# Kernel tuning notes

Hardware: AMD Instinct MI355X
Metric: run time of the kernel (lower is better)

Reference implementation:

```python
import jax, jax.numpy as jnp
import numpy as np

L, H, D, DH, F = 2, 12, 768, 64, 3072
B, T = 2, 2048
LN_EPS = 1e-5


def setup_inputs() -> dict:
    key = jax.random.key(0)
    ks = jax.random.split(key, 16)
    s = 0.02
    inp = {
        "x": jax.random.normal(ks[0], (B, T, D), dtype=jnp.float32),
        "attn_mask": jnp.ones((1, T, T), dtype=jnp.int32),
        # per-layer, per-head QKV projections
        "Wq": jax.random.normal(ks[1], (L, H, D, DH), jnp.float32) * s,
        "bq": jnp.zeros((L, H, DH), jnp.float32),
        "Wk": jax.random.normal(ks[2], (L, H, D, DH), jnp.float32) * s,
        "bk": jnp.zeros((L, H, DH), jnp.float32),
        "Wv": jax.random.normal(ks[3], (L, H, D, DH), jnp.float32) * s,
        "bv": jnp.zeros((L, H, DH), jnp.float32),
        # output projection over concatenated heads
        "Wo": jax.random.normal(ks[4], (L, H * DH, D), jnp.float32) * s,
        "bo": jnp.zeros((L, D), jnp.float32),
        # FFN: LayerNorm -> Linear -> GELU -> Linear
        "ln_g": jnp.ones((L, D), jnp.float32),
        "ln_b": jnp.zeros((L, D), jnp.float32),
        "W1": jax.random.normal(ks[5], (L, D, F), jnp.float32) * s,
        "b1": jnp.zeros((L, F), jnp.float32),
        "W2": jax.random.normal(ks[6], (L, F, D), jnp.float32) * s,
        "b2": jnp.zeros((L, D), jnp.float32),
    }
    return inp


def _layer(x, mask, Wq, bq, Wk, bk, Wv, bv, Wo, bo, ln_g, ln_b, W1, b1, W2, b2):
    # batched multi-head attention (equivalent to per-head loop in source)
    q = jnp.einsum("btd,hde->bhte", x, Wq) + bq[None, :, None, :]
    k = jnp.einsum("btd,hde->bhte", x, Wk) + bk[None, :, None, :]
    v = jnp.einsum("btd,hde->bhte", x, Wv) + bv[None, :, None, :]
    scores = jnp.einsum("bhte,bhse->bhts", q, k) / np.sqrt(DH).astype(np.float32)
    scores = jnp.where(mask[:, None, :, :] == 0, -jnp.inf, scores)
    alpha = jax.nn.softmax(scores, axis=-1)
    attn = jnp.einsum("bhts,bhse->bhte", alpha, v)  # [B,H,T,DH]
    concat = attn.transpose(0, 2, 1, 3).reshape(x.shape[0], x.shape[1], H * DH)
    x = concat @ Wo + bo + x  # attention residual
    # FFN with pre-LayerNorm inside the block, residual around it
    mu = jnp.mean(x, axis=-1, keepdims=True)
    var = jnp.mean(jnp.square(x - mu), axis=-1, keepdims=True)
    h = (x - mu) * jax.lax.rsqrt(var + LN_EPS) * ln_g + ln_b
    h = jax.nn.gelu(h @ W1 + b1, approximate=False) @ W2 + b2
    return h + x


def reference(x, attn_mask, Wq, bq, Wk, bk, Wv, bv, Wo, bo, ln_g, ln_b, W1, b1, W2, b2):
    for l in range(L):
        x = _layer(x, attn_mask,
                   Wq[l], bq[l], Wk[l], bk[l], Wv[l], bv[l],
                   Wo[l], bo[l], ln_g[l], ln_b[l],
                   W1[l], b1[l], W2[l], b2[l])
    return x
```

## Files before the change

kernel.cpp:

```cpp
#include <hip/hip_runtime.h>
#include <math.h>

#define CL 2
#define CH 12
#define CD 768
#define CDH 64
#define CF 3072
#define CB 2
#define CT 2048
#define CBTCD ((size_t)CB * CT * CD)

typedef __bf16 bf16x8 __attribute__((ext_vector_type(8)));
typedef float f32x4 __attribute__((ext_vector_type(4)));
typedef short s16x4 __attribute__((ext_vector_type(4)));
typedef ushort u16x4 __attribute__((ext_vector_type(4)));

#define QSCALE 0.18033688011112042f

__device__ __forceinline__ ushort f2bf(float f) {
  return __builtin_bit_cast(ushort, (__bf16)f);
}

__device__ __forceinline__ float fexp2(float x) {
  float r;
  asm volatile("v_exp_f32 %0, %1" : "=v"(r) : "v"(x));
  return r;
}

__device__ __forceinline__ float wred_sum(float v) {
#pragma unroll
  for (int o = 32; o > 0; o >>= 1) v += __shfl_xor(v, o);
  return v;
}

__device__ __forceinline__ void gload16(const ushort* g, ushort* l) {
  __builtin_amdgcn_global_load_lds(
      (const __attribute__((address_space(1))) unsigned int*)g,
      (__attribute__((address_space(3))) unsigned int*)l, 16, 0, 0);
}

enum { EPI_BF16 = 1, EPI_BIAS_BF16 = 2, EPI_BIAS_GELU_BF16 = 3, EPI_BIAS_RES_F32 = 4, EPI_BIAS_RES_F32_BF16 = 5, EPI_PART_F32 = 6 };

template <int EPI>
__global__ __launch_bounds__(256) void gemm_k(
    const ushort* __restrict__ A, int lda,
    const ushort* __restrict__ B, int ldb,
    void* __restrict__ Cv, int ldc,
    int K,
    const float* __restrict__ bias,
    const float* __restrict__ res,
    ushort* __restrict__ C2) {
  __shared__ ushort As[2][128 * 32];
  __shared__ ushort Bs[2][128 * 32];
  const int tid = threadIdx.x;
  const int lane = tid & 63;
  const int wave = tid >> 6;
  const int wm = (wave >> 1) * 64;
  const int wn = (wave & 1) * 64;

  const int gx = gridDim.x;
  const int nwg = gx * gridDim.y;
  int wgid = blockIdx.y * gx + blockIdx.x;
  const int cpx = nwg >> 3;
  wgid = (wgid & 7) * cpx + (wgid >> 3);
  const int m0 = (wgid / gx) * 128;
  const int n0 = (wgid % gx) * 128;

  const int lr = lane & 15;
  const int lg = lane >> 4;
  f32x4 acc[4][4] = {};

  const int kz = blockIdx.z * K;
  const ushort* pa = A + (size_t)(m0 + (tid >> 2)) * lda + (tid & 3) * 8 + kz;
  const ushort* pb = B + (size_t)(n0 + (tid >> 2)) * ldb + (tid & 3) * 8 + kz;

  auto stage = [&](int buf, int k0) {
#pragma unroll
    for (int p = 0; p < 2; ++p) {
      gload16(pa + (size_t)p * 64 * lda + k0, &As[buf][wave * 512 + p * 2048]);
      gload16(pb + (size_t)p * 64 * ldb + k0, &Bs[buf][wave * 512 + p * 2048]);
    }
  };

  const int nt = K >> 5;
  stage(0, 0);
  for (int kt = 0; kt < nt; ++kt) {
    const int cur = kt & 1;
    if (kt + 1 < nt) {
      stage(cur ^ 1, (kt + 1) << 5);
      asm volatile("s_waitcnt vmcnt(4)" ::: "memory");
    } else {
      asm volatile("s_waitcnt vmcnt(0)" ::: "memory");
    }
    __builtin_amdgcn_s_barrier();
    __builtin_amdgcn_sched_barrier(0);

    bf16x8 af[4], bfr[4];
#pragma unroll
    for (int f = 0; f < 4; ++f) af[f] = *(const bf16x8*)(&As[cur][(wm + f * 16 + lr) * 32 + lg * 8]);
#pragma unroll
    for (int f = 0; f < 4; ++f) bfr[f] = *(const bf16x8*)(&Bs[cur][(wn + f * 16 + lr) * 32 + lg * 8]);
#pragma unroll
    for (int i = 0; i < 4; ++i)
#pragma unroll
      for (int j = 0; j < 4; ++j)
        acc[i][j] = __builtin_amdgcn_mfma_f32_16x16x32_bf16(af[i], bfr[j], acc[i][j], 0, 0, 0);

    __builtin_amdgcn_sched_barrier(0);
    __builtin_amdgcn_s_barrier();
  }

  const int cr0 = lg * 4;
#pragma unroll
  for (int i = 0; i < 4; ++i) {
#pragma unroll
    for (int j = 0; j < 4; ++j) {
      int col = n0 + wn + j * 16 + lr;
#pragma unroll
      for (int r = 0; r < 4; ++r) {
        int row = m0 + wm + i * 16 + cr0 + r;
        float val = acc[i][j][r];
        size_t offc = (size_t)row * ldc + col;
        if constexpr (EPI == EPI_BF16) {
          ((ushort*)Cv)[offc] = f2bf(val);
        } else if constexpr (EPI == EPI_BIAS_BF16) {
          ((ushort*)Cv)[offc] = f2bf(val + bias[col]);
        } else if constexpr (EPI == EPI_BIAS_GELU_BF16) {
          float x = val + bias[col];
          float gel = 0.5f * x * (1.0f + erff(x * 0.70710678118654752f));
          ((ushort*)Cv)[offc] = f2bf(gel);
        } else if constexpr (EPI == EPI_BIAS_RES_F32) {
          ((float*)Cv)[offc] = val + bias[col] + res[offc];
        } else if constexpr (EPI == EPI_PART_F32) {
          ((float*)Cv)[blockIdx.z * CBTCD + offc] = val;
        } else {
          float o = val + bias[col] + res[offc];
          ((float*)Cv)[offc] = o;
          C2[offc] = f2bf(o);
        }
      }
    }
  }
}

template <bool DUAL>
__global__ __launch_bounds__(256) void reduce2_k(const float* __restrict__ part,
                                                 const float* __restrict__ bias,
                                                 const float* __restrict__ res,
                                                 float* __restrict__ outf,
                                                 ushort* __restrict__ outb) {
  int i = blockIdx.x * 256 + threadIdx.x;
  float4 p0 = ((const float4*)part)[i];
  float4 p1 = ((const float4*)(part + CBTCD))[i];
  float4 rr = ((const float4*)res)[i];
  int col = (i * 4) % CD;
  float4 bb = *(const float4*)(bias + col);
  float4 o;
  o.x = p0.x + p1.x + rr.x + bb.x;
  o.y = p0.y + p1.y + rr.y + bb.y;
  o.z = p0.z + p1.z + rr.z + bb.z;
  o.w = p0.w + p1.w + rr.w + bb.w;
  ((float4*)outf)[i] = o;
  if constexpr (DUAL) {
    ushort4 u;
    u.x = f2bf(o.x); u.y = f2bf(o.y); u.z = f2bf(o.z); u.w = f2bf(o.w);
    ((ushort4*)outb)[i] = u;
  }
}

__global__ __launch_bounds__(256) void flash_k(const ushort* __restrict__ qkv,
                                               const ushort* __restrict__ vt,
                                               const unsigned* __restrict__ mbits,
                                               ushort* __restrict__ out) {
  const int q0 = blockIdx.x * 64;
  const int bh = blockIdx.y;
  const int b = bh / CH, h = bh % CH;
  const int tid = threadIdx.x;
  const int lane = tid & 63;
  const int wave = tid >> 6;
  const int lr = lane & 15;
  const int lg = lane >> 4;

  __shared__ ushort Ks[64][72];
  __shared__ ushort Vt[64][72];

  const int qg = q0 + wave * 16 + lr;
  const ushort* qrow = qkv + ((size_t)(b * CT) + qg) * 2304 + h * CDH;
  bf16x8 aq0 = *(const bf16x8*)(qrow + lg * 8);
  bf16x8 aq1 = *(const bf16x8*)(qrow + 32 + lg * 8);

  f32x4 acc[4] = {};
  float m_run = -1e30f, l_run = 0.f;

  const ushort* kbase = qkv + (size_t)(b * CT) * 2304 + CD + h * CDH;
  const ushort* vbase = vt + (size_t)bh * 64 * CT;

  const int r0 = tid >> 3, r1 = 32 + (tid >> 3), cc = (tid & 7) * 8;

  auto ld = [&](int kv0, bf16x8& k0, bf16x8& k1, bf16x8& v0, bf16x8& v1) {
    k0 = *(const bf16x8*)(kbase + (size_t)(kv0 + r0) * 2304 + cc);
    k1 = *(const bf16x8*)(kbase + (size_t)(kv0 + r1) * 2304 + cc);
    v0 = *(const bf16x8*)(vbase + (size_t)r0 * CT + kv0 + cc);
    v1 = *(const bf16x8*)(vbase + (size_t)r1 * CT + kv0 + cc);
  };
  auto st = [&](bf16x8 k0, bf16x8 k1, bf16x8 v0, bf16x8 v1) {
    *(bf16x8*)(&Ks[r0][cc]) = k0;
    *(bf16x8*)(&Ks[r1][cc]) = k1;
    *(bf16x8*)(&Vt[r0][cc]) = v0;
    *(bf16x8*)(&Vt[r1][cc]) = v1;
  };

  auto compute = [&](int kv0) {
    f32x4 stt[4];
    __builtin_amdgcn_s_setprio(1);
#pragma unroll
    for (int j = 0; j < 4; ++j) {
      bf16x8 kf0 = *(const bf16x8*)(&Ks[j * 16 + lr][lg * 8]);
      bf16x8 kf1 = *(const bf16x8*)(&Ks[j * 16 + lr][32 + lg * 8]);
      f32x4 t = {};
      t = __builtin_amdgcn_mfma_f32_16x16x32_bf16(kf0, aq0, t, 0, 0, 0);
      t = __builtin_amdgcn_mfma_f32_16x16x32_bf16(kf1, aq1, t, 0, 0, 0);
      stt[j] = t;
    }
    __builtin_amdgcn_s_setprio(0);

    unsigned w0 = mbits[(size_t)qg * 64 + (kv0 >> 5)];
    unsigned w1 = mbits[(size_t)qg * 64 + (kv0 >> 5) + 1];
    float tmax = -INFINITY;
    if ((w0 & w1) == 0xFFFFFFFFu) {
#pragma unroll
      for (int j = 0; j < 4; ++j)
#pragma unroll
        for (int r = 0; r < 4; ++r) tmax = fmaxf(tmax, stt[j][r]);
    } else {
#pragma unroll
      for (int j = 0; j < 4; ++j) {
        unsigned w = (j < 2) ? w0 : w1;
#pragma unroll
        for (int r = 0; r < 4; ++r) {
          int bit = (j * 16 + lg * 4 + r) & 31;
          if (((w >> bit) & 1u) == 0u) stt[j][r] = -INFINITY;
          tmax = fmaxf(tmax, stt[j][r]);
        }
      }
    }
    tmax = fmaxf(tmax, __shfl_xor(tmax, 16));
    tmax = fmaxf(tmax, __shfl_xor(tmax, 32));

    if (__any(tmax - m_run > 8.0f)) {
      float mnew = fmaxf(m_run, tmax);
      float sc = fexp2(m_run - mnew);
      m_run = mnew;
      l_run *= sc;
#pragma unroll
      for (int jj = 0; jj < 4; ++jj) {
        acc[jj][0] *= sc; acc[jj][1] *= sc; acc[jj][2] *= sc; acc[jj][3] *= sc;
      }
    }

    s16x4 pf[4];
#pragma unroll
    for (int j = 0; j < 4; ++j) {
      s16x4 pv;
#pragma unroll
      for (int r = 0; r < 4; ++r) {
        float p = fexp2(stt[j][r] - m_run);
        l_run += p;
        pv[r] = (short)f2bf(p);
      }
      pf[j] = pv;
    }

    __builtin_amdgcn_s_setprio(1);
#pragma unroll
    for (int jj = 0; jj < 4; ++jj) {
#pragma unroll
      for (int j = 0; j < 4; ++j) {
        s16x4 vf = *(const s16x4*)(&Vt[jj * 16 + lr][j * 16 + lg * 4]);
        acc[jj] = __builtin_amdgcn_mfma_f32_16x16x16bf16_1k(vf, pf[j], acc[jj], 0, 0, 0);
      }
    }
    __builtin_amdgcn_s_setprio(0);
  };

  bf16x8 ka0, ka1, va0, va1, kb0, kb1, vb0, vb1;
  ld(0, ka0, ka1, va0, va1);
  for (int kv0 = 0; kv0 < CT; kv0 += 128) {
    __syncthreads();
    st(ka0, ka1, va0, va1);
    __syncthreads();
    ld(kv0 + 64, kb0, kb1, vb0, vb1);
    compute(kv0);
    __syncthreads();
    st(kb0, kb1, vb0, vb1);
    __syncthreads();
    if (kv0 + 128 < CT) ld(kv0 + 128, ka0, ka1, va0, va1);
    compute(kv0 + 64);
  }

  l_run += __shfl_xor(l_run, 16);
  l_run += __shfl_xor(l_run, 32);

  float inv = 1.0f / l_run;
  const int orow = b * CT + qg;
#pragma unroll
  for (int jj = 0; jj < 4; ++jj) {
    u16x4 o;
#pragma unroll
    for (int r = 0; r < 4; ++r) o[r] = f2bf(acc[jj][r] * inv);
    *(u16x4*)(out + (size_t)orow * CD + h * CDH + jj * 16 + lg * 4) = o;
  }
}

__global__ __launch_bounds__(256) void vtrans_k(const ushort* __restrict__ qkv,
                                                ushort* __restrict__ vt) {
  const int t0 = blockIdx.x * 64;
  const int bh = blockIdx.y;
  const int b = bh / CH, h = bh % CH;
  const int tid = threadIdx.x;
  __shared__ ushort tile[64][72];
#pragma unroll
  for (int p = 0; p < 2; ++p) {
    int i = p * 2048 + tid * 8;
    int tr = i >> 6, c = i & 63;
    *(bf16x8*)(&tile[tr][c]) =
        *(const bf16x8*)(qkv + (size_t)(b * CT + t0 + tr) * 2304 + 2 * CD + h * CDH + c);
  }
  __syncthreads();
#pragma unroll
  for (int p = 0; p < 2; ++p) {
    int i = p * 2048 + tid * 8;
    int er = i >> 6, tc = i & 63;
    ushort tmp[8];
#pragma unroll
    for (int j = 0; j < 8; ++j) tmp[j] = tile[tc + j][er];
    *(bf16x8*)(vt + (size_t)bh * 64 * CT + (size_t)er * CT + t0 + tc) = *(bf16x8*)tmp;
  }
}

__global__ void maskbits_k(const int* __restrict__ mask, unsigned* __restrict__ mbits) {
  int idx = blockIdx.x * 256 + threadIdx.x;
  if (idx >= CT * 64) return;
  const int* mp = mask + (size_t)(idx >> 6) * CT + (idx & 63) * 32;
  unsigned bits = 0;
#pragma unroll
  for (int j = 0; j < 32; ++j) bits |= (mp[j] != 0 ? 1u : 0u) << j;
  mbits[idx] = bits;
}

__global__ __launch_bounds__(256) void ln_k(const float* __restrict__ X,
                                            ushort* __restrict__ H,
                                            const float* __restrict__ g,
                                            const float* __restrict__ b) {
  const int t = blockIdx.x;
  const int tid = threadIdx.x;
  const float* row = X + (size_t)t * CD;
  float x0 = row[tid], x1 = row[tid + 256], x2 = row[tid + 512];
  float s = wred_sum(x0 + x1 + x2);
  __shared__ float sh[4], sh2[4];
  if ((tid & 63) == 0) sh[tid >> 6] = s;
  __syncthreads();
  float mu = (sh[0] + sh[1] + sh[2] + sh[3]) * (1.0f / 768.0f);
  float d0 = x0 - mu, d1 = x1 - mu, d2 = x2 - mu;
  float vs = wred_sum(d0 * d0 + d1 * d1 + d2 * d2);
  if ((tid & 63) == 0) sh2[tid >> 6] = vs;
  __syncthreads();
  float var = (sh2[0] + sh2[1] + sh2[2] + sh2[3]) * (1.0f / 768.0f);
  float r = 1.0f / sqrtf(var + 1e-5f);
  H[(size_t)t * CD + tid] = f2bf(d0 * r * g[tid] + b[tid]);
  H[(size_t)t * CD + tid + 256] = f2bf(d1 * r * g[tid + 256] + b[tid + 256]);
  H[(size_t)t * CD + tid + 512] = f2bf(d2 * r * g[tid + 512] + b[tid + 512]);
}

__global__ void f32_to_bf16_k(const float* __restrict__ in, ushort* __restrict__ out, int n4) {
  int i = blockIdx.x * 256 + threadIdx.x;
  if (i >= n4) return;
  float4 f = *(const float4*)(in + (size_t)i * 4);
  ushort4 u;
  u.x = f2bf(f.x); u.y = f2bf(f.y); u.z = f2bf(f.z); u.w = f2bf(f.w);
  *(ushort4*)(out + (size_t)i * 4) = u;
}

__global__ __launch_bounds__(256) void tcvt_k(const float* __restrict__ src, size_t sbs,
                                              ushort* __restrict__ dst, size_t dbs,
                                              int R, int C, float scale) {
  __shared__ float t[32][33];
  const float* s = src + blockIdx.z * sbs;
  ushort* d = dst + blockIdx.z * dbs;
  const int tx = threadIdx.x & 31;
  const int ty4 = (threadIdx.x >> 5) * 4;
  const int r0 = blockIdx.y * 32, c0 = blockIdx.x * 32;
#pragma unroll
  for (int i = 0; i < 4; ++i) t[ty4 + i][tx] = s[(size_t)(r0 + ty4 + i) * C + c0 + tx];
  __syncthreads();
#pragma unroll
  for (int i = 0; i < 4; ++i)
    d[(size_t)(c0 + ty4 + i) * R + r0 + tx] = f2bf(t[tx][ty4 + i] * scale);
}

__global__ void repack_bqkv_k(const float* __restrict__ bq, const float* __restrict__ bk,
                              const float* __restrict__ bv, float* __restrict__ dst) {
  int idx = blockIdx.x * 256 + threadIdx.x;
  if (idx >= CL * 2304) return;
  int l = idx / 2304;
  int c = idx % 2304;
  int sec = c / CD;
  int within = c % CD;
  int h = within / CDH;
  int e = within % CDH;
  const float* B = (sec == 0) ? bq : ((sec == 1) ? bk : bv);
  float v = B[((size_t)l * CH + h) * CDH + e];
  if (sec == 0) v *= QSCALE;
  dst[idx] = v;
}

extern "C" void kernel_launch(void* const* d_in, const int* in_sizes, int n_in,
                              void* d_out, int out_size, void* d_ws, size_t ws_size,
                              hipStream_t stream) {
  (void)in_sizes; (void)n_in; (void)out_size; (void)ws_size;
  const float* X = (const float*)d_in[0];
  const int* MSK = (const int*)d_in[1];
  const float* Wq = (const float*)d_in[2];
  const float* bq = (const float*)d_in[3];
  const float* Wk = (const float*)d_in[4];
  const float* bk = (const float*)d_in[5];
  const float* Wv = (const float*)d_in[6];
  const float* bv = (const float*)d_in[7];
  const float* Wo = (const float*)d_in[8];
  const float* bo = (const float*)d_in[9];
  const float* lng = (const float*)d_in[10];
  const float* lnb = (const float*)d_in[11];
  const float* W1 = (const float*)d_in[12];
  const float* b1 = (const float*)d_in[13];
  const float* W2 = (const float*)d_in[14];
  const float* b2 = (const float*)d_in[15];

  char* base = (char*)d_ws;
  size_t off = 0;
  auto alloc = [&](size_t bytes) {
    char* p = base + off;
    off = (off + bytes + 255) & ~(size_t)255;
    return p;
  };
  ushort* wqkv_t = (ushort*)alloc((size_t)CL * 2304 * CD * 2);
  ushort* wo_t = (ushort*)alloc((size_t)CL * CD * CD * 2);
  ushort* w1_t = (ushort*)alloc((size_t)CL * CF * CD * 2);
  ushort* w2_t = (ushort*)alloc((size_t)CL * CD * CF * 2);
  float* bqkv = (float*)alloc((size_t)CL * 2304 * 4);
  ushort* xb = (ushort*)alloc((size_t)CB * CT * CD * 2);
  ushort* qkv = (ushort*)alloc((size_t)CB * CT * 2304 * 2);
  ushort* vt = (ushort*)alloc((size_t)CB * CH * CDH * CT * 2);
  unsigned* mbits = (unsigned*)alloc((size_t)CT * 64 * 4);
  ushort* attno = (ushort*)alloc((size_t)CB * CT * CD * 2);
  float* xattn = (float*)alloc((size_t)CB * CT * CD * 4);
  float* xf = (float*)alloc((size_t)CB * CT * CD * 4);
  ushort* hln = (ushort*)alloc((size_t)CB * CT * CD * 2);
  ushort* gbuf = (ushort*)alloc((size_t)CB * CT * CF * 2);
  float* part = (float*)qkv;

  const int BT_ = CB * CT;

  for (int l = 0; l < CL; ++l) {
    tcvt_k<<<dim3(CDH / 32, CD / 32, CH), 256, 0, stream>>>(
        Wq + (size_t)l * CH * CD * CDH, (size_t)CD * CDH,
        wqkv_t + (size_t)l * 2304 * CD + 0 * CD * CD, (size_t)CDH * CD,
        CD, CDH, QSCALE);
    tcvt_k<<<dim3(CDH / 32, CD / 32, CH), 256, 0, stream>>>(
        Wk + (size_t)l * CH * CD * CDH, (size_t)CD * CDH,
        wqkv_t + (size_t)l * 2304 * CD + 1 * CD * CD, (size_t)CDH * CD,
        CD, CDH, 1.0f);
    tcvt_k<<<dim3(CDH / 32, CD / 32, CH), 256, 0, stream>>>(
        Wv + (size_t)l * CH * CD * CDH, (size_t)CD * CDH,
        wqkv_t + (size_t)l * 2304 * CD + 2 * CD * CD, (size_t)CDH * CD,
        CD, CDH, 1.0f);
  }
  tcvt_k<<<dim3(CD / 32, CD / 32, CL), 256, 0, stream>>>(
      Wo, (size_t)CD * CD, wo_t, (size_t)CD * CD, CD, CD, 1.0f);
  tcvt_k<<<dim3(CF / 32, CD / 32, CL), 256, 0, stream>>>(
      W1, (size_t)CD * CF, w1_t, (size_t)CF * CD, CD, CF, 1.0f);
  tcvt_k<<<dim3(CD / 32, CF / 32, CL), 256, 0, stream>>>(
      W2, (size_t)CF * CD, w2_t, (size_t)CD * CF, CF, CD, 1.0f);
  {
    int n = CL * 2304;
    repack_bqkv_k<<<(n + 255) / 256, 256, 0, stream>>>(bq, bk, bv, bqkv);
  }
  maskbits_k<<<(CT * 64 + 255) / 256, 256, 0, stream>>>(MSK, mbits);

  {
    int n4 = BT_ * CD / 4;
    f32_to_bf16_k<<<(n4 + 255) / 256, 256, 0, stream>>>(X, xb, n4);
  }

  for (int l = 0; l < CL; ++l) {
    const float* xcur = (l == 0) ? X : xf;
    gemm_k<EPI_BIAS_BF16><<<dim3(2304 / 128, BT_ / 128), 256, 0, stream>>>(
        xb, CD, wqkv_t + (size_t)l * 2304 * CD, CD, qkv, 2304, CD,
        bqkv + (size_t)l * 2304, nullptr, nullptr);
    vtrans_k<<<dim3(CT / 64, CB * CH), 256, 0, stream>>>(qkv, vt);
    flash_k<<<dim3(CT / 64, CB * CH), 256, 0, stream>>>(qkv, vt, mbits, attno);
    gemm_k<EPI_BIAS_RES_F32><<<dim3(CD / 128, BT_ / 128), 256, 0, stream>>>(
        attno, CD, wo_t + (size_t)l * CD * CD, CD, xattn, CD, CD,
        bo + (size_t)l * CD, xcur, nullptr);
    ln_k<<<BT_, 256, 0, stream>>>(xattn, hln, lng + (size_t)l * CD, lnb + (size_t)l * CD);
    gemm_k<EPI_BIAS_GELU_BF16><<<dim3(CF / 128, BT_ / 128), 256, 0, stream>>>(
        hln, CD, w1_t + (size_t)l * CF * CD, CD, gbuf, CF, CD,
        b1 + (size_t)l * CF, nullptr, nullptr);
    gemm_k<EPI_PART_F32><<<dim3(CD / 128, BT_ / 128, 2), 256, 0, stream>>>(
        gbuf, CF, w2_t + (size_t)l * CD * CF, CF, part, CD, CF / 2,
        nullptr, nullptr, nullptr);
    const int nred = BT_ * CD / 4 / 256;
    if (l == CL - 1) {
      reduce2_k<false><<<nred, 256, 0, stream>>>(part, b2 + (size_t)l * CD, xattn,
                                                 (float*)d_out, nullptr);
    } else {
      reduce2_k<true><<<nred, 256, 0, stream>>>(part, b2 + (size_t)l * CD, xattn,
                                                xf, xb);
    }
  }
}
```

Before: 438.5 us.

## Split flash attention along KV into two halves with merge kernel

Flash attention now runs a two-way split over the key/value sequence (grid z=2), writing unnormalized fp32 partial outputs plus running max and sum to scratch, and a new merge kernel combines the halves and writes bf16. This doubles the number of blocks (768 vs 384) to fill more CUs, at the cost of extra fp32 traffic and one more launch. The partial output buffer reuses the GELU buffer, which is free at that point.

```diff
diff --git a/kernel.cpp b/kernel.cpp
--- a/kernel.cpp
+++ b/kernel.cpp
@@ -8,6 +8,7 @@
 #define CF 3072
 #define CB 2
 #define CT 2048
+#define CBH (CB * CH)
 #define CBTCD ((size_t)CB * CT * CD)
 
 typedef __bf16 bf16x8 __attribute__((ext_vector_type(8)));
@@ -171,15 +172,18 @@
 __global__ __launch_bounds__(256) void flash_k(const ushort* __restrict__ qkv,
                                                const ushort* __restrict__ vt,
                                                const unsigned* __restrict__ mbits,
-                                               ushort* __restrict__ out) {
+                                               float* __restrict__ Opart,
+                                               float2* __restrict__ ml) {
   const int q0 = blockIdx.x * 64;
   const int bh = blockIdx.y;
+  const int z = blockIdx.z;
   const int b = bh / CH, h = bh % CH;
   const int tid = threadIdx.x;
   const int lane = tid & 63;
   const int wave = tid >> 6;
   const int lr = lane & 15;
   const int lg = lane >> 4;
+  const int KVH = CT / 2;
 
   __shared__ ushort Ks[64][72];
   __shared__ ushort Vt[64][72];
@@ -192,8 +196,8 @@
   f32x4 acc[4] = {};
   float m_run = -1e30f, l_run = 0.f;
 
-  const ushort* kbase = qkv + (size_t)(b * CT) * 2304 + CD + h * CDH;
-  const ushort* vbase = vt + (size_t)bh * 64 * CT;
+  const ushort* kbase = qkv + ((size_t)(b * CT) + (size_t)z * KVH) * 2304 + CD + h * CDH;
+  const ushort* vbase = vt + (size_t)bh * 64 * CT + (size_t)z * KVH;
 
   const int r0 = tid >> 3, r1 = 32 + (tid >> 3), cc = (tid & 7) * 8;
 
@@ -224,8 +228,9 @@
     }
     __builtin_amdgcn_s_setprio(0);
 
-    unsigned w0 = mbits[(size_t)qg * 64 + (kv0 >> 5)];
-    unsigned w1 = mbits[(size_t)qg * 64 + (kv0 >> 5) + 1];
+    const int kglob = z * KVH + kv0;
+    unsigned w0 = mbits[(size_t)qg * 64 + (kglob >> 5)];
+    unsigned w1 = mbits[(size_t)qg * 64 + (kglob >> 5) + 1];
     float tmax = -INFINITY;
     if ((w0 & w1) == 0xFFFFFFFFu) {
 #pragma unroll
@@ -285,7 +290,7 @@
 
   bf16x8 ka0, ka1, va0, va1, kb0, kb1, vb0, vb1;
   ld(0, ka0, ka1, va0, va1);
-  for (int kv0 = 0; kv0 < CT; kv0 += 128) {
+  for (int kv0 = 0; kv0 < KVH; kv0 += 128) {
     __syncthreads();
     st(ka0, ka1, va0, va1);
     __syncthreads();
@@ -294,22 +299,41 @@
     __syncthreads();
     st(kb0, kb1, vb0, vb1);
     __syncthreads();
-    if (kv0 + 128 < CT) ld(kv0 + 128, ka0, ka1, va0, va1);
+    if (kv0 + 128 < KVH) ld(kv0 + 128, ka0, ka1, va0, va1);
     compute(kv0 + 64);
   }
 
   l_run += __shfl_xor(l_run, 16);
   l_run += __shfl_xor(l_run, 32);
 
-  float inv = 1.0f / l_run;
-  const int orow = b * CT + qg;
-#pragma unroll
-  for (int jj = 0; jj < 4; ++jj) {
-    u16x4 o;
-#pragma unroll
-    for (int r = 0; r < 4; ++r) o[r] = f2bf(acc[jj][r] * inv);
-    *(u16x4*)(out + (size_t)orow * CD + h * CDH + jj * 16 + lg * 4) = o;
-  }
+  const size_t obase = (((size_t)z * CBH + bh) * CT + qg) * 64;
+#pragma unroll
+  for (int jj = 0; jj < 4; ++jj)
+    *(f32x4*)(Opart + obase + jj * 16 + lg * 4) = acc[jj];
+  if (lg == 0) ml[((size_t)z * CBH + bh) * CT + qg] = make_float2(m_run, l_run);
+}
+
+__global__ __launch_bounds__(256) void merge_k(const float* __restrict__ Opart,
+                                               const float2* __restrict__ ml,
+                                               ushort* __restrict__ out) {
+  int i = blockIdx.x * 256 + threadIdx.x;
+  int e0 = (i & 15) * 4;
+  int t = (i >> 4) & (CT - 1);
+  int bh = i >> 15;
+  int b = bh / CH, h = bh % CH;
+  float2 a = ml[(size_t)bh * CT + t];
+  float2 c = ml[((size_t)CBH + bh) * CT + t];
+  float m = fmaxf(a.x, c.x);
+  float w0 = fexp2(a.x - m), w1 = fexp2(c.x - m);
+  float inv = 1.0f / (a.y * w0 + c.y * w1);
+  float4 o0 = *(const float4*)(Opart + ((size_t)bh * CT + t) * 64 + e0);
+  float4 o1 = *(const float4*)(Opart + (((size_t)CBH + bh) * CT + t) * 64 + e0);
+  u16x4 o;
+  o[0] = f2bf((o0.x * w0 + o1.x * w1) * inv);
+  o[1] = f2bf((o0.y * w0 + o1.y * w1) * inv);
+  o[2] = f2bf((o0.z * w0 + o1.z * w1) * inv);
+  o[3] = f2bf((o0.w * w0 + o1.w * w1) * inv);
+  *(u16x4*)(out + ((size_t)b * CT + t) * CD + h * CDH + e0) = o;
 }
 
 __global__ __launch_bounds__(256) void vtrans_k(const ushort* __restrict__ qkv,
@@ -456,7 +480,9 @@
   float* xf = (float*)alloc((size_t)CB * CT * CD * 4);
   ushort* hln = (ushort*)alloc((size_t)CB * CT * CD * 2);
   ushort* gbuf = (ushort*)alloc((size_t)CB * CT * CF * 2);
+  float2* ml = (float2*)alloc((size_t)2 * CBH * CT * 8);
   float* part = (float*)qkv;
+  float* Opart = (float*)gbuf;
 
   const int BT_ = CB * CT;
 
@@ -496,8 +522,9 @@
     gemm_k<EPI_BIAS_BF16><<<dim3(2304 / 128, BT_ / 128), 256, 0, stream>>>(
         xb, CD, wqkv_t + (size_t)l * 2304 * CD, CD, qkv, 2304, CD,
         bqkv + (size_t)l * 2304, nullptr, nullptr);
-    vtrans_k<<<dim3(CT / 64, CB * CH), 256, 0, stream>>>(qkv, vt);
-    flash_k<<<dim3(CT / 64, CB * CH), 256, 0, stream>>>(qkv, vt, mbits, attno);
+    vtrans_k<<<dim3(CT / 64, CBH), 256, 0, stream>>>(qkv, vt);
+    flash_k<<<dim3(CT / 64, CBH, 2), 256, 0, stream>>>(qkv, vt, mbits, Opart, ml);
+    merge_k<<<CBH * CT * 16 / 256, 256, 0, stream>>>(Opart, ml, attno);
     gemm_k<EPI_BIAS_RES_F32><<<dim3(CD / 128, BT_ / 128), 256, 0, stream>>>(
         attno, CD, wo_t + (size_t)l * CD * CD, CD, xattn, CD, CD,
         bo + (size_t)l * CD, xcur, nullptr);
```

New measurement: 453.6 us. 3.4% more time.

## Fuse V transpose into QKV GEMM epilogue and triple-buffer GEMM LDS staging

Applied to the files above, without the earlier changes.

The QKV GEMM gets a dedicated epilogue that writes the V columns straight into the transposed per-head layout the flash kernel reads. This removes the separate vtrans kernel launch and its extra read and write of V. Separately, every GEMM now uses three LDS stages with prefetch distance two instead of double buffering, so more loads are in flight. The cost is 50% more shared memory per block, which may lower occupancy, and V stores of 4 contiguous bf16 that are less coalesced.

```diff
diff --git a/kernel.cpp b/kernel.cpp
--- a/kernel.cpp
+++ b/kernel.cpp
@@ -8,6 +8,7 @@
 #define CF 3072
 #define CB 2
 #define CT 2048
+#define CBH (CB * CH)
 #define CBTCD ((size_t)CB * CT * CD)
 
 typedef __bf16 bf16x8 __attribute__((ext_vector_type(8)));
@@ -39,7 +40,7 @@
       (__attribute__((address_space(3))) unsigned int*)l, 16, 0, 0);
 }
 
-enum { EPI_BF16 = 1, EPI_BIAS_BF16 = 2, EPI_BIAS_GELU_BF16 = 3, EPI_BIAS_RES_F32 = 4, EPI_BIAS_RES_F32_BF16 = 5, EPI_PART_F32 = 6 };
+enum { EPI_BF16 = 1, EPI_BIAS_BF16 = 2, EPI_BIAS_GELU_BF16 = 3, EPI_BIAS_RES_F32 = 4, EPI_BIAS_RES_F32_BF16 = 5, EPI_PART_F32 = 6, EPI_QKV = 7 };
 
 template <int EPI>
 __global__ __launch_bounds__(256) void gemm_k(
@@ -50,8 +51,8 @@
     const float* __restrict__ bias,
     const float* __restrict__ res,
     ushort* __restrict__ C2) {
-  __shared__ ushort As[2][128 * 32];
-  __shared__ ushort Bs[2][128 * 32];
+  __shared__ ushort As[3][128 * 32];
+  __shared__ ushort Bs[3][128 * 32];
   const int tid = threadIdx.x;
   const int lane = tid & 63;
   const int wave = tid >> 6;
@@ -84,10 +85,13 @@
 
   const int nt = K >> 5;
   stage(0, 0);
+  stage(1, 32);
   for (int kt = 0; kt < nt; ++kt) {
-    const int cur = kt & 1;
-    if (kt + 1 < nt) {
-      stage(cur ^ 1, (kt + 1) << 5);
+    const int cur = kt % 3;
+    if (kt + 2 < nt) {
+      stage((kt + 2) % 3, (kt + 2) << 5);
+      asm volatile("s_waitcnt vmcnt(8)" ::: "memory");
+    } else if (kt + 1 < nt) {
       asm volatile("s_waitcnt vmcnt(4)" ::: "memory");
     } else {
       asm volatile("s_waitcnt vmcnt(0)" ::: "memory");
@@ -116,6 +120,26 @@
 #pragma unroll
     for (int j = 0; j < 4; ++j) {
       int col = n0 + wn + j * 16 + lr;
+      if constexpr (EPI == EPI_QKV) {
+        const int cbase = n0 + wn + j * 16;
+        const int row0 = m0 + wm + i * 16 + cr0;
+        float bcol = bias[col];
+        if (cbase >= 2 * CD) {
+          const int bb = row0 >> 11;
+          const int t0 = row0 & (CT - 1);
+          const int hh = (cbase - 2 * CD) >> 6;
+          const int ee = ((cbase - 2 * CD) & 63) + lr;
+          u16x4 o;
+#pragma unroll
+          for (int r = 0; r < 4; ++r) o[r] = f2bf(acc[i][j][r] + bcol);
+          *(u16x4*)(C2 + ((size_t)(bb * CH + hh) * 64 + ee) * CT + t0) = o;
+        } else {
+#pragma unroll
+          for (int r = 0; r < 4; ++r)
+            ((ushort*)Cv)[(size_t)(row0 + r) * ldc + col] = f2bf(acc[i][j][r] + bcol);
+        }
+        continue;
+      }
 #pragma unroll
       for (int r = 0; r < 4; ++r) {
         int row = m0 + wm + i * 16 + cr0 + r;
@@ -133,7 +157,7 @@
           ((float*)Cv)[offc] = val + bias[col] + res[offc];
         } else if constexpr (EPI == EPI_PART_F32) {
           ((float*)Cv)[blockIdx.z * CBTCD + offc] = val;
-        } else {
+        } else if constexpr (EPI == EPI_BIAS_RES_F32_BF16) {
           float o = val + bias[col] + res[offc];
           ((float*)Cv)[offc] = o;
           C2[offc] = f2bf(o);
@@ -312,32 +336,6 @@
   }
 }
 
-__global__ __launch_bounds__(256) void vtrans_k(const ushort* __restrict__ qkv,
-                                                ushort* __restrict__ vt) {
-  const int t0 = blockIdx.x * 64;
-  const int bh = blockIdx.y;
-  const int b = bh / CH, h = bh % CH;
-  const int tid = threadIdx.x;
-  __shared__ ushort tile[64][72];
-#pragma unroll
-  for (int p = 0; p < 2; ++p) {
-    int i = p * 2048 + tid * 8;
-    int tr = i >> 6, c = i & 63;
-    *(bf16x8*)(&tile[tr][c]) =
-        *(const bf16x8*)(qkv + (size_t)(b * CT + t0 + tr) * 2304 + 2 * CD + h * CDH + c);
-  }
-  __syncthreads();
-#pragma unroll
-  for (int p = 0; p < 2; ++p) {
-    int i = p * 2048 + tid * 8;
-    int er = i >> 6, tc = i & 63;
-    ushort tmp[8];
-#pragma unroll
-    for (int j = 0; j < 8; ++j) tmp[j] = tile[tc + j][er];
-    *(bf16x8*)(vt + (size_t)bh * 64 * CT + (size_t)er * CT + t0 + tc) = *(bf16x8*)tmp;
-  }
-}
-
 __global__ void maskbits_k(const int* __restrict__ mask, unsigned* __restrict__ mbits) {
   int idx = blockIdx.x * 256 + threadIdx.x;
   if (idx >= CT * 64) return;
@@ -493,11 +491,10 @@
 
   for (int l = 0; l < CL; ++l) {
     const float* xcur = (l == 0) ? X : xf;
-    gemm_k<EPI_BIAS_BF16><<<dim3(2304 / 128, BT_ / 128), 256, 0, stream>>>(
+    gemm_k<EPI_QKV><<<dim3(2304 / 128, BT_ / 128), 256, 0, stream>>>(
         xb, CD, wqkv_t + (size_t)l * 2304 * CD, CD, qkv, 2304, CD,
-        bqkv + (size_t)l * 2304, nullptr, nullptr);
-    vtrans_k<<<dim3(CT / 64, CB * CH), 256, 0, stream>>>(qkv, vt);
-    flash_k<<<dim3(CT / 64, CB * CH), 256, 0, stream>>>(qkv, vt, mbits, attno);
+        bqkv + (size_t)l * 2304, nullptr, vt);
+    flash_k<<<dim3(CT / 64, CBH), 256, 0, stream>>>(qkv, vt, mbits, attno);
     gemm_k<EPI_BIAS_RES_F32><<<dim3(CD / 128, BT_ / 128), 256, 0, stream>>>(
         attno, CD, wo_t + (size_t)l * CD * CD, CD, xattn, CD, CD,
         bo + (size_t)l * CD, xcur, nullptr);
```

Result: no change. 431.7 us (-1.5%).
